# Kernel tuning notes

Hardware: AMD Instinct MI355X
Metric: run time of the kernel (lower is better)

The kernel has to match this reference:

```python
import jax, jax.numpy as jnp
import numpy as np

GROUPS = 32
NUM_HEADS = 8
EPS = 1e-5


def setup_inputs() -> dict:
    key = jax.random.key(0)
    ks = jax.random.split(key, 8)
    b, c, h, w = 2, 256, 64, 64
    x = jax.random.normal(ks[0], (b, c, h, w), dtype=jnp.float32)
    gn_w = jnp.ones((c,), dtype=jnp.float32)
    gn_b = jnp.zeros((c,), dtype=jnp.float32)
    qkv_w = jax.random.normal(ks[1], (3 * c, c), dtype=jnp.float32) * 0.02  # 1x1 conv
    qkv_b = jnp.zeros((3 * c,), dtype=jnp.float32)
    proj_w = jax.random.normal(ks[2], (c, c), dtype=jnp.float32) * 0.02  # 1x1 conv
    proj_b = jnp.zeros((c,), dtype=jnp.float32)
    return {"x": x, "gn_w": gn_w, "gn_b": gn_b, "qkv_w": qkv_w,
            "qkv_b": qkv_b, "proj_w": proj_w, "proj_b": proj_b}


def _group_norm(x, w, b):
    bsz, c, h, wd = x.shape
    xg = x.reshape(bsz, GROUPS, c // GROUPS, h * wd)
    mean = jnp.mean(xg, axis=(2, 3), keepdims=True)
    var = jnp.mean(jnp.square(xg - mean), axis=(2, 3), keepdims=True)
    xn = ((xg - mean) * jax.lax.rsqrt(var + EPS)).reshape(bsz, c, h, wd)
    return xn * w[None, :, None, None] + b[None, :, None, None]


def reference(x, gn_w, gn_b, qkv_w, qkv_b, proj_w, proj_b):
    b, c, h, w = x.shape
    hd = c // NUM_HEADS
    s = h * w
    xn = _group_norm(x, gn_w, gn_b)
    # 1x1 conv == channel matmul
    qkv = jnp.einsum('oc,bcs->bos', qkv_w, xn.reshape(b, c, s)) + qkv_b[None, :, None]
    qkv = qkv.reshape(b, 3, NUM_HEADS, hd, s)
    q, k, v = qkv[:, 0], qkv[:, 1], qkv[:, 2]  # (b, nh, hd, s)
    scale = 1.0 / jnp.sqrt(jnp.asarray(hd, dtype=x.dtype))
    scores = jnp.einsum('bhds,bhdt->bhst', q, k) * scale  # (b, nh, s, s)
    attn = jax.nn.softmax(scores, axis=-1)
    out = jnp.einsum('bhst,bhdt->bhds', attn, v)  # (b, nh, hd, s)
    out = out.reshape(b, c, h, w)
    out = jnp.einsum('oc,bcs->bos', proj_w, out.reshape(b, c, s)).reshape(b, c, h, w)
    out = out + proj_b[None, :, None, None]
    return out + x
```

## Files before the change

kernel.cpp:

```cpp
#include <hip/hip_runtime.h>
#include <hip/hip_bf16.h>

#define B_ 2
#define C_ 256
#define S_ 4096
#define NH 8
#define HD 32
#define EPSV 1e-5f
#define QSC2 0.25503487942324256f

typedef __bf16 bf16_t;
typedef bf16_t bf16x8 __attribute__((ext_vector_type(8)));
typedef float f32x4 __attribute__((ext_vector_type(4)));
typedef float f32x16 __attribute__((ext_vector_type(16)));
typedef int i32x2 __attribute__((ext_vector_type(2)));
typedef __hip_bfloat16 hbf;

__device__ inline unsigned cvtpk_bf16(float a, float b) {
  unsigned r;
  asm("v_cvt_pk_bf16_f32 %0, %1, %2" : "=v"(r) : "v"(a), "v"(b));
  return r;
}

#if __has_builtin(__builtin_amdgcn_exp2f)
#define EXP2R(x) __builtin_amdgcn_exp2f(x)
#else
#define EXP2R(x) exp2f(x)
#endif

__global__ __launch_bounds__(256) void f2bf_kernel(const float* __restrict__ src, hbf* __restrict__ dst, int n) {
  int i = blockIdx.x * 256 + threadIdx.x;
  if (i < n) dst[i] = __float2bfloat16(src[i]);
}

__global__ __launch_bounds__(256) void wfrag_kernel(const float* __restrict__ src, hbf* __restrict__ dst, int nchunks) {
  int i = blockIdx.x * 256 + threadIdx.x;
  if (i >= nchunks) return;
  int o = i >> 5, c8 = (i & 31) * 8;
  alignas(16) hbf tmp[8];
#pragma unroll
  for (int j = 0; j < 8; j++) tmp[j] = __float2bfloat16(src[(size_t)o * C_ + c8 + j]);
  *(uint4*)&dst[(((size_t)(o >> 5) * 16) + (c8 >> 4)) * 512 + (o & 31) * 16 + (c8 & 15)] = *(uint4*)tmp;
}

__global__ __launch_bounds__(256) void gn_stats(const float* __restrict__ x, float* __restrict__ stats) {
  int bg = blockIdx.x >> 3, chunk = blockIdx.x & 7;
  const float4* xp4 = (const float4*)(x + (size_t)bg * 8 * S_);
  float sum = 0.f, sumsq = 0.f;
#pragma unroll
  for (int p = 0; p < 4; p++) {
    int i = threadIdx.x + p * 256;
    int ch = i >> 7, s4 = i & 127;
    float4 v = xp4[ch * (S_ >> 2) + chunk * 128 + s4];
    sum += v.x + v.y + v.z + v.w;
    sumsq += v.x * v.x + v.y * v.y + v.z * v.z + v.w * v.w;
  }
#pragma unroll
  for (int off = 32; off > 0; off >>= 1) {
    sum += __shfl_down(sum, off);
    sumsq += __shfl_down(sumsq, off);
  }
  __shared__ float red[2][4];
  int wid = threadIdx.x >> 6;
  if ((threadIdx.x & 63) == 0) { red[0][wid] = sum; red[1][wid] = sumsq; }
  __syncthreads();
  if (threadIdx.x == 0) {
    stats[blockIdx.x * 2 + 0] = red[0][0] + red[0][1] + red[0][2] + red[0][3];
    stats[blockIdx.x * 2 + 1] = red[1][0] + red[1][1] + red[1][2] + red[1][3];
  }
}

__global__ __launch_bounds__(256) void gn_apply(const float* __restrict__ x, const float* __restrict__ gw,
                                                const float* __restrict__ gb, const float* __restrict__ stats,
                                                hbf* __restrict__ xn) {
  int bg = blockIdx.x >> 3, chunk = blockIdx.x & 7;
  int b = bg >> 5, g = bg & 31;
  const float* xp = x + (size_t)bg * 8 * S_;
  float sum = 0.f, sumsq = 0.f;
#pragma unroll
  for (int k = 0; k < 8; k++) {
    sum += stats[(bg * 8 + k) * 2 + 0];
    sumsq += stats[(bg * 8 + k) * 2 + 1];
  }
  const float inv_n = 1.f / (8 * S_);
  float mean = sum * inv_n;
  float rstd = rsqrtf(fmaxf(sumsq * inv_n - mean * mean, 0.f) + EPSV);
  float scv[8], shv[8];
#pragma unroll
  for (int c = 0; c < 8; c++) {
    scv[c] = gw[g * 8 + c] * rstd;
    shv[c] = gb[g * 8 + c] - mean * scv[c];
  }
#pragma unroll
  for (int p = 0; p < 2; p++) {
    int s = chunk * 512 + p * 256 + threadIdx.x;
    alignas(16) hbf tmp[8];
#pragma unroll
    for (int c = 0; c < 8; c++)
      tmp[c] = __float2bfloat16(xp[(size_t)c * S_ + s] * scv[c] + shv[c]);
    *(uint4*)&xn[(((size_t)b * (S_ >> 5) + (s >> 5)) * 16 + (g >> 1)) * 512 + (s & 31) * 16 + (g & 1) * 8] =
        *(uint4*)tmp;
  }
}

__global__ __launch_bounds__(512, 4) void qkv_gemm(const hbf* __restrict__ xn, const hbf* __restrict__ wf,
                                                   const float* __restrict__ bias,
                                                   hbf* __restrict__ qbuf, hbf* __restrict__ kg,
                                                   hbf* __restrict__ vg) {
  int bt = blockIdx.z;
  int m0 = blockIdx.x * 128;
  int n0 = blockIdx.y * 128;
  int tid = threadIdx.x, lane = tid & 63, w = tid >> 6;
  int wq = w & 3, wo = w >> 2;
  int l31 = lane & 31, hi = lane >> 5;
  const int loff = l31 * 16 + hi * 8;
  const hbf* ap = xn + ((size_t)bt * (S_ >> 5) + (m0 >> 5) + wq) * 8192;
  int oc0 = n0 + wo * 64;
  const hbf* bp0 = wf + (size_t)(oc0 >> 5) * 8192;
  const hbf* bp1 = bp0 + 8192;
  f32x16 acc0 = {0.f,0.f,0.f,0.f,0.f,0.f,0.f,0.f,0.f,0.f,0.f,0.f,0.f,0.f,0.f,0.f};
  f32x16 acc1 = acc0;
#pragma unroll 4
  for (int ks = 0; ks < 16; ++ks) {
    bf16x8 af = *(const bf16x8*)(ap + ks * 512 + loff);
    bf16x8 b0 = *(const bf16x8*)(bp0 + ks * 512 + loff);
    bf16x8 b1 = *(const bf16x8*)(bp1 + ks * 512 + loff);
    acc0 = __builtin_amdgcn_mfma_f32_32x32x16_bf16(af, b0, acc0, 0, 0, 0);
    acc1 = __builtin_amdgcn_mfma_f32_32x32x16_bf16(af, b1, acc1, 0, 0, 0);
  }
  int s_base = m0 + wq * 32;
#pragma unroll
  for (int ct = 0; ct < 2; ++ct) {
    f32x16 a = ct ? acc1 : acc0;
    int oc = oc0 + ct * 32;
    int o = oc + l31;
    float bs = bias[o];
    if (oc < 256) {
#pragma unroll
      for (int r = 0; r < 16; r++) {
        int s = s_base + (r & 3) + 8 * (r >> 2) + 4 * hi;
        qbuf[((size_t)bt * S_ + s) * C_ + o] = __float2bfloat16((a[r] + bs) * QSC2);
      }
    } else if (oc < 512) {
      int hh = (oc - 256) >> 5;
      const size_t khead = (size_t)(bt * NH + hh) * (S_ >> 5);
#pragma unroll
      for (int r = 0; r < 16; r++) {
        int s = s_base + (r & 3) + 8 * (r >> 2) + 4 * hi;
        kg[(khead + (s >> 5)) * 1024 + (l31 >> 4) * 512 + (s & 31) * 16 + (l31 & 15)] =
            __float2bfloat16(a[r] + bs);
      }
    } else {
      int hh = (oc - 512) >> 5;
      const size_t vhead = (size_t)(bt * NH + hh) * (S_ >> 4);
#pragma unroll
      for (int r = 0; r < 16; r++) {
        int s = s_base + (r & 3) + 8 * (r >> 2) + 4 * hi;
        vg[(vhead + (s >> 4)) * 512 + l31 * 16 + (s & 15)] = __float2bfloat16(a[r] + bs);
      }
    }
  }
}

__device__ inline void softmax_pv(f32x16 sc, bf16x8 va0, bf16x8 va1,
                                  f32x16& o_acc, float& l_run) {
#pragma unroll
  for (int i = 0; i < 16; i++) sc[i] = EXP2R(sc[i]);
  {
    float s0a = sc[0] + sc[1], s1a = sc[2] + sc[3], s2a = sc[4] + sc[5], s3a = sc[6] + sc[7];
    float s4a = sc[8] + sc[9], s5a = sc[10] + sc[11], s6a = sc[12] + sc[13], s7a = sc[14] + sc[15];
    s0a += s1a; s2a += s3a; s4a += s5a; s6a += s7a;
    s0a += s2a; s4a += s6a;
    l_run += s0a + s4a;
  }
#pragma unroll
  for (int kb = 0; kb < 2; kb++) {
    unsigned a0 = cvtpk_bf16(sc[kb * 8 + 0], sc[kb * 8 + 1]);
    unsigned b0 = cvtpk_bf16(sc[kb * 8 + 2], sc[kb * 8 + 3]);
    unsigned a1 = cvtpk_bf16(sc[kb * 8 + 4], sc[kb * 8 + 5]);
    unsigned b1 = cvtpk_bf16(sc[kb * 8 + 6], sc[kb * 8 + 7]);
    i32x2 ra = __builtin_amdgcn_permlane32_swap((int)a0, (int)a1, false, false);
    i32x2 rb = __builtin_amdgcn_permlane32_swap((int)b0, (int)b1, false, false);
    union { unsigned u[4]; bf16x8 v; } pf;
    pf.u[0] = (unsigned)ra[0]; pf.u[1] = (unsigned)rb[0];
    pf.u[2] = (unsigned)ra[1]; pf.u[3] = (unsigned)rb[1];
    o_acc = __builtin_amdgcn_mfma_f32_32x32x16_bf16(kb ? va1 : va0, pf.v, o_acc, 0, 0, 0);
  }
}

__global__ __launch_bounds__(512, 4) void attn_kernel(const hbf* __restrict__ qbuf, const hbf* __restrict__ kg,
                                                      const hbf* __restrict__ vg, hbf* __restrict__ attn_t) {
  int bid = blockIdx.x;
  int xcd = bid & 7, idx = bid >> 3;
  int combo = (xcd << 1) | (idx >> 6);
  int bt = combo >> 3, h = combo & 7;
  int s0 = (idx & 63) << 6;
  int tid = threadIdx.x, lane = tid & 63, w = tid >> 6;
  int wq = w & 1, wt = w >> 1;
  int l31 = lane & 31, hi = lane >> 5;
  const int loff = (l31 << 4) + (hi << 3);
  int qrow = s0 + wq * 32 + l31;
  bf16x8 qf0 = *(const bf16x8*)&qbuf[((size_t)bt * S_ + qrow) * C_ + h * HD + hi * 8];
  bf16x8 qf1 = *(const bf16x8*)&qbuf[((size_t)bt * S_ + qrow) * C_ + h * HD + 16 + hi * 8];
  f32x16 o_acc = {0.f,0.f,0.f,0.f,0.f,0.f,0.f,0.f,0.f,0.f,0.f,0.f,0.f,0.f,0.f,0.f};
  const f32x16 z16 = o_acc;
  float l_run = 0.f;
  const int tq0 = wt << 10;
  const hbf* kq = kg + ((size_t)(bt * NH + h) * (S_ >> 5) + (tq0 >> 5)) * 1024;
  const hbf* vq = vg + ((size_t)(bt * NH + h) * (S_ >> 4) + (tq0 >> 4)) * 512;
  bf16x8 kaB0 = *(const bf16x8*)(kq + loff);
  bf16x8 kaB1 = *(const bf16x8*)(kq + loff + 512);
  f32x16 scA = __builtin_amdgcn_mfma_f32_32x32x16_bf16(kaB0, qf0, z16, 0, 0, 0);
  scA = __builtin_amdgcn_mfma_f32_32x32x16_bf16(kaB1, qf1, scA, 0, 0, 0);
  kaB0 = *(const bf16x8*)(kq + loff + 1024);
  kaB1 = *(const bf16x8*)(kq + loff + 1536);
  bf16x8 vaA0 = *(const bf16x8*)(vq + loff);
  bf16x8 vaA1 = *(const bf16x8*)(vq + loff + 512);
  kq += 2048;
  vq += 1024;
  for (int j = 0; j < 15; ++j) {
    bf16x8 vaB0 = *(const bf16x8*)(vq + loff);
    bf16x8 vaB1 = *(const bf16x8*)(vq + loff + 512);
    bf16x8 knA0 = *(const bf16x8*)(kq + loff);
    bf16x8 knA1 = *(const bf16x8*)(kq + loff + 512);
    f32x16 scB = __builtin_amdgcn_mfma_f32_32x32x16_bf16(kaB0, qf0, z16, 0, 0, 0);
    scB = __builtin_amdgcn_mfma_f32_32x32x16_bf16(kaB1, qf1, scB, 0, 0, 0);
    kaB0 = *(const bf16x8*)(kq + loff + 1024);
    kaB1 = *(const bf16x8*)(kq + loff + 1536);
    softmax_pv(scA, vaA0, vaA1, o_acc, l_run);
    vaA0 = *(const bf16x8*)(vq + loff + 1024);
    vaA1 = *(const bf16x8*)(vq + loff + 1536);
    scA = __builtin_amdgcn_mfma_f32_32x32x16_bf16(knA0, qf0, z16, 0, 0, 0);
    scA = __builtin_amdgcn_mfma_f32_32x32x16_bf16(knA1, qf1, scA, 0, 0, 0);
    softmax_pv(scB, vaB0, vaB1, o_acc, l_run);
    kq += 2048; vq += 2048;
  }
  {
    bf16x8 vaB0 = *(const bf16x8*)(vq + loff);
    bf16x8 vaB1 = *(const bf16x8*)(vq + loff + 512);
    f32x16 scB = __builtin_amdgcn_mfma_f32_32x32x16_bf16(kaB0, qf0, z16, 0, 0, 0);
    scB = __builtin_amdgcn_mfma_f32_32x32x16_bf16(kaB1, qf1, scB, 0, 0, 0);
    softmax_pv(scA, vaA0, vaA1, o_acc, l_run);
    softmax_pv(scB, vaB0, vaB1, o_acc, l_run);
  }
  __shared__ f32x16 ored[6 * 64];
  __shared__ float lred[8 * 64];
  __syncthreads();
  lred[(w << 6) + lane] = l_run;
  if (wt > 0) ored[((w - 2) << 6) + lane] = o_acc;
  __syncthreads();
  if (wt == 0) {
    float l_tot = 0.f;
#pragma unroll
    for (int k = 0; k < 4; k++) {
      int wp = wq + 2 * k;
      l_tot += lred[(wp << 6) + l31] + lred[(wp << 6) + 32 + l31];
    }
    f32x16 o = o_acc;
#pragma unroll
    for (int k = 0; k < 3; k++) {
      f32x16 t2 = ored[((wq + 2 * k) << 6) + lane];
#pragma unroll
      for (int i = 0; i < 16; i++) o[i] += t2[i];
    }
    float inv_l = 1.0f / l_tot;
#pragma unroll
    for (int c2 = 0; c2 < 4; c2++) {
      alignas(8) hbf tmp[4];
#pragma unroll
      for (int r = 0; r < 4; r++) tmp[r] = __float2bfloat16(o[c2 * 4 + r] * inv_l);
      *(uint2*)&attn_t[((size_t)bt * S_ + qrow) * C_ + h * HD + c2 * 8 + hi * 4] = *(uint2*)tmp;
    }
  }
}

__global__ __launch_bounds__(256) void proj_gemm(const hbf* __restrict__ attn_t, const hbf* __restrict__ wb,
                                                 const float* __restrict__ bias, const float* __restrict__ x,
                                                 float* __restrict__ out) {
  int bt = blockIdx.z;
  int m0 = blockIdx.x * 64;
  int n0 = blockIdx.y * 64;
  const hbf* A = attn_t + (size_t)bt * S_ * C_;
  __shared__ hbf a_lds[64][72];
  __shared__ hbf b_lds[64][72];
  int tid = threadIdx.x, lane = tid & 63, wid = tid >> 6;
  int wm = (wid >> 1) * 32, wn = (wid & 1) * 32;
  f32x4 acc[2][2] = {};
  for (int k0 = 0; k0 < C_; k0 += 64) {
    __syncthreads();
    int r = tid >> 3, kk = (tid & 7) * 8;
#pragma unroll
    for (int p = 0; p < 2; p++) {
      *(bf16x8*)&a_lds[r + p * 32][kk] = *(const bf16x8*)&A[(size_t)(m0 + r + p * 32) * C_ + k0 + kk];
      *(bf16x8*)&b_lds[r + p * 32][kk] = *(const bf16x8*)&wb[(size_t)(n0 + r + p * 32) * C_ + k0 + kk];
    }
    __syncthreads();
#pragma unroll
    for (int kk2 = 0; kk2 < 64; kk2 += 32) {
      bf16x8 af[2], bfr[2];
#pragma unroll
      for (int mi = 0; mi < 2; mi++)
        af[mi] = *(const bf16x8*)&a_lds[wm + mi * 16 + (lane & 15)][kk2 + (lane >> 4) * 8];
#pragma unroll
      for (int ni = 0; ni < 2; ni++)
        bfr[ni] = *(const bf16x8*)&b_lds[wn + ni * 16 + (lane & 15)][kk2 + (lane >> 4) * 8];
#pragma unroll
      for (int mi = 0; mi < 2; mi++)
#pragma unroll
        for (int ni = 0; ni < 2; ni++)
          acc[mi][ni] = __builtin_amdgcn_mfma_f32_16x16x32_bf16(af[mi], bfr[ni], acc[mi][ni], 0, 0, 0);
    }
  }
#pragma unroll
  for (int mi = 0; mi < 2; mi++)
#pragma unroll
    for (int ni = 0; ni < 2; ni++) {
      int o = n0 + wn + ni * 16 + (lane & 15);
      int s = m0 + wm + mi * 16 + (lane >> 4) * 4;
      size_t base = ((size_t)bt * C_ + o) * S_ + s;
      float pb = bias[o];
      float4 xr = *(const float4*)&x[base];
      float4 res;
      res.x = acc[mi][ni][0] + pb + xr.x;
      res.y = acc[mi][ni][1] + pb + xr.y;
      res.z = acc[mi][ni][2] + pb + xr.z;
      res.w = acc[mi][ni][3] + pb + xr.w;
      *(float4*)&out[base] = res;
    }
}

extern "C" void kernel_launch(void* const* d_in, const int* in_sizes, int n_in,
                              void* d_out, int out_size, void* d_ws, size_t ws_size,
                              hipStream_t stream) {
  const float* x = (const float*)d_in[0];
  const float* gn_w = (const float*)d_in[1];
  const float* gn_b = (const float*)d_in[2];
  const float* qkv_w = (const float*)d_in[3];
  const float* qkv_b = (const float*)d_in[4];
  const float* proj_w = (const float*)d_in[5];
  const float* proj_b = (const float*)d_in[6];
  float* out = (float*)d_out;

  hbf* qkv_wf = (hbf*)d_ws;
  hbf* proj_w_bf = qkv_wf + 768 * 256;
  hbf* xn = proj_w_bf + 256 * 256;
  hbf* qbuf = xn + (size_t)B_ * S_ * C_;
  hbf* kg = qbuf + (size_t)B_ * S_ * C_;
  hbf* vg = kg + (size_t)B_ * S_ * C_;
  hbf* attn_t = vg + (size_t)B_ * S_ * C_;
  float* stats = (float*)(attn_t + (size_t)B_ * S_ * C_);

  dim3 blk(256);
  wfrag_kernel<<<(768 * 32 + 255) / 256, blk, 0, stream>>>(qkv_w, qkv_wf, 768 * 32);
  f2bf_kernel<<<(256 * 256 + 255) / 256, blk, 0, stream>>>(proj_w, proj_w_bf, 256 * 256);
  gn_stats<<<512, blk, 0, stream>>>(x, stats);
  gn_apply<<<512, blk, 0, stream>>>(x, gn_w, gn_b, stats, xn);
  qkv_gemm<<<dim3(32, 6, 2), dim3(512), 0, stream>>>(xn, qkv_wf, qkv_b, qbuf, kg, vg);
  attn_kernel<<<dim3(1024), dim3(512), 0, stream>>>(qbuf, kg, vg, attn_t);
  proj_gemm<<<dim3(64, 4, 2), blk, 0, stream>>>(attn_t, proj_w_bf, proj_b, x, out);
}
```

Baseline: 83.28 us.

## Merge weight prep and GN stats into one kernel; LDS-free proj GEMM with fragment-ordered weights

Fuses the qkv weight fragment conversion, the projection weight conversion and the group-norm statistics into a single launch, removing two kernel launches. The projection weights are now stored in the same fragment-major layout as the qkv weights. proj_gemm drops its LDS staging and barriers and feeds 32x32x16 MFMAs straight from global memory. This cuts launch overhead and LDS/sync cost, but the epilogue now does scalar, lane-strided stores and x reads instead of float4, which may hurt coalescing.

```diff
diff --git a/kernel.cpp b/kernel.cpp
--- a/kernel.cpp
+++ b/kernel.cpp
@@ -28,23 +28,28 @@
 #define EXP2R(x) exp2f(x)
 #endif
 
-__global__ __launch_bounds__(256) void f2bf_kernel(const float* __restrict__ src, hbf* __restrict__ dst, int n) {
-  int i = blockIdx.x * 256 + threadIdx.x;
-  if (i < n) dst[i] = __float2bfloat16(src[i]);
-}
-
-__global__ __launch_bounds__(256) void wfrag_kernel(const float* __restrict__ src, hbf* __restrict__ dst, int nchunks) {
-  int i = blockIdx.x * 256 + threadIdx.x;
-  if (i >= nchunks) return;
-  int o = i >> 5, c8 = (i & 31) * 8;
-  alignas(16) hbf tmp[8];
-#pragma unroll
-  for (int j = 0; j < 8; j++) tmp[j] = __float2bfloat16(src[(size_t)o * C_ + c8 + j]);
-  *(uint4*)&dst[(((size_t)(o >> 5) * 16) + (c8 >> 4)) * 512 + (o & 31) * 16 + (c8 & 15)] = *(uint4*)tmp;
-}
-
-__global__ __launch_bounds__(256) void gn_stats(const float* __restrict__ x, float* __restrict__ stats) {
-  int bg = blockIdx.x >> 3, chunk = blockIdx.x & 7;
+__global__ __launch_bounds__(256) void prep_kernel(const float* __restrict__ qkv_w,
+                                                   const float* __restrict__ proj_w,
+                                                   const float* __restrict__ x,
+                                                   hbf* __restrict__ qkv_wf, hbf* __restrict__ proj_wf,
+                                                   float* __restrict__ stats) {
+  int blk = blockIdx.x;
+  if (blk < 128) {
+    const float* src = (blk < 96) ? qkv_w : proj_w;
+    hbf* dst = (blk < 96) ? qkv_wf : proj_wf;
+    int i = (blk < 96 ? blk : blk - 96) * 256 + threadIdx.x;
+    int nchunks = (blk < 96) ? 768 * 32 : 256 * 32;
+    if (i < nchunks) {
+      int o = i >> 5, c8 = (i & 31) * 8;
+      alignas(16) hbf tmp[8];
+#pragma unroll
+      for (int j = 0; j < 8; j++) tmp[j] = __float2bfloat16(src[(size_t)o * C_ + c8 + j]);
+      *(uint4*)&dst[(((size_t)(o >> 5) * 16) + (c8 >> 4)) * 512 + (o & 31) * 16 + (c8 & 15)] = *(uint4*)tmp;
+    }
+    return;
+  }
+  int sb = blk - 128;
+  int bg = sb >> 3, chunk = sb & 7;
   const float4* xp4 = (const float4*)(x + (size_t)bg * 8 * S_);
   float sum = 0.f, sumsq = 0.f;
 #pragma unroll
@@ -65,8 +70,8 @@
   if ((threadIdx.x & 63) == 0) { red[0][wid] = sum; red[1][wid] = sumsq; }
   __syncthreads();
   if (threadIdx.x == 0) {
-    stats[blockIdx.x * 2 + 0] = red[0][0] + red[0][1] + red[0][2] + red[0][3];
-    stats[blockIdx.x * 2 + 1] = red[1][0] + red[1][1] + red[1][2] + red[1][3];
+    stats[sb * 2 + 0] = red[0][0] + red[0][1] + red[0][2] + red[0][3];
+    stats[sb * 2 + 1] = red[1][0] + red[1][1] + red[1][2] + red[1][3];
   }
 }
 
@@ -274,59 +279,34 @@
   }
 }
 
-__global__ __launch_bounds__(256) void proj_gemm(const hbf* __restrict__ attn_t, const hbf* __restrict__ wb,
+__global__ __launch_bounds__(256) void proj_gemm(const hbf* __restrict__ attn_t, const hbf* __restrict__ wf,
                                                  const float* __restrict__ bias, const float* __restrict__ x,
                                                  float* __restrict__ out) {
   int bt = blockIdx.z;
-  int m0 = blockIdx.x * 64;
-  int n0 = blockIdx.y * 64;
-  const hbf* A = attn_t + (size_t)bt * S_ * C_;
-  __shared__ hbf a_lds[64][72];
-  __shared__ hbf b_lds[64][72];
-  int tid = threadIdx.x, lane = tid & 63, wid = tid >> 6;
-  int wm = (wid >> 1) * 32, wn = (wid & 1) * 32;
-  f32x4 acc[2][2] = {};
-  for (int k0 = 0; k0 < C_; k0 += 64) {
-    __syncthreads();
-    int r = tid >> 3, kk = (tid & 7) * 8;
-#pragma unroll
-    for (int p = 0; p < 2; p++) {
-      *(bf16x8*)&a_lds[r + p * 32][kk] = *(const bf16x8*)&A[(size_t)(m0 + r + p * 32) * C_ + k0 + kk];
-      *(bf16x8*)&b_lds[r + p * 32][kk] = *(const bf16x8*)&wb[(size_t)(n0 + r + p * 32) * C_ + k0 + kk];
-    }
-    __syncthreads();
-#pragma unroll
-    for (int kk2 = 0; kk2 < 64; kk2 += 32) {
-      bf16x8 af[2], bfr[2];
-#pragma unroll
-      for (int mi = 0; mi < 2; mi++)
-        af[mi] = *(const bf16x8*)&a_lds[wm + mi * 16 + (lane & 15)][kk2 + (lane >> 4) * 8];
-#pragma unroll
-      for (int ni = 0; ni < 2; ni++)
-        bfr[ni] = *(const bf16x8*)&b_lds[wn + ni * 16 + (lane & 15)][kk2 + (lane >> 4) * 8];
-#pragma unroll
-      for (int mi = 0; mi < 2; mi++)
-#pragma unroll
-        for (int ni = 0; ni < 2; ni++)
-          acc[mi][ni] = __builtin_amdgcn_mfma_f32_16x16x32_bf16(af[mi], bfr[ni], acc[mi][ni], 0, 0, 0);
-    }
-  }
-#pragma unroll
-  for (int mi = 0; mi < 2; mi++)
-#pragma unroll
-    for (int ni = 0; ni < 2; ni++) {
-      int o = n0 + wn + ni * 16 + (lane & 15);
-      int s = m0 + wm + mi * 16 + (lane >> 4) * 4;
-      size_t base = ((size_t)bt * C_ + o) * S_ + s;
-      float pb = bias[o];
-      float4 xr = *(const float4*)&x[base];
-      float4 res;
-      res.x = acc[mi][ni][0] + pb + xr.x;
-      res.y = acc[mi][ni][1] + pb + xr.y;
-      res.z = acc[mi][ni][2] + pb + xr.z;
-      res.w = acc[mi][ni][3] + pb + xr.w;
-      *(float4*)&out[base] = res;
-    }
+  int s_blk = blockIdx.x * 64;
+  int o_blk = blockIdx.y * 64;
+  int tid = threadIdx.x, lane = tid & 63, w = tid >> 6;
+  int wo = w & 1, ws = w >> 1;
+  int l31 = lane & 31, hi = lane >> 5;
+  const int loff = l31 * 16 + hi * 8;
+  int o0 = o_blk + wo * 32;
+  int s0 = s_blk + ws * 32;
+  const hbf* ap = wf + (size_t)(o0 >> 5) * 8192;
+  const hbf* bp = attn_t + ((size_t)bt * S_ + s0 + l31) * C_ + hi * 8;
+  f32x16 acc = {0.f,0.f,0.f,0.f,0.f,0.f,0.f,0.f,0.f,0.f,0.f,0.f,0.f,0.f,0.f,0.f};
+#pragma unroll 4
+  for (int ks = 0; ks < 16; ++ks) {
+    bf16x8 af = *(const bf16x8*)(ap + ks * 512 + loff);
+    bf16x8 bf_ = *(const bf16x8*)(bp + ks * 16);
+    acc = __builtin_amdgcn_mfma_f32_32x32x16_bf16(af, bf_, acc, 0, 0, 0);
+  }
+  int s = s0 + l31;
+#pragma unroll
+  for (int r = 0; r < 16; r++) {
+    int o = o0 + (r & 3) + 8 * (r >> 2) + 4 * hi;
+    size_t idx = ((size_t)bt * C_ + o) * S_ + s;
+    out[idx] = acc[r] + bias[o] + x[idx];
+  }
 }
 
 extern "C" void kernel_launch(void* const* d_in, const int* in_sizes, int n_in,
@@ -342,8 +322,8 @@
   float* out = (float*)d_out;
 
   hbf* qkv_wf = (hbf*)d_ws;
-  hbf* proj_w_bf = qkv_wf + 768 * 256;
-  hbf* xn = proj_w_bf + 256 * 256;
+  hbf* proj_wf = qkv_wf + 768 * 256;
+  hbf* xn = proj_wf + 256 * 256;
   hbf* qbuf = xn + (size_t)B_ * S_ * C_;
   hbf* kg = qbuf + (size_t)B_ * S_ * C_;
   hbf* vg = kg + (size_t)B_ * S_ * C_;
@@ -351,11 +331,9 @@
   float* stats = (float*)(attn_t + (size_t)B_ * S_ * C_);
 
   dim3 blk(256);
-  wfrag_kernel<<<(768 * 32 + 255) / 256, blk, 0, stream>>>(qkv_w, qkv_wf, 768 * 32);
-  f2bf_kernel<<<(256 * 256 + 255) / 256, blk, 0, stream>>>(proj_w, proj_w_bf, 256 * 256);
-  gn_stats<<<512, blk, 0, stream>>>(x, stats);
+  prep_kernel<<<640, blk, 0, stream>>>(qkv_w, proj_w, x, qkv_wf, proj_wf, stats);
   gn_apply<<<512, blk, 0, stream>>>(x, gn_w, gn_b, stats, xn);
   qkv_gemm<<<dim3(32, 6, 2), dim3(512), 0, stream>>>(xn, qkv_wf, qkv_b, qbuf, kg, vg);
   attn_kernel<<<dim3(1024), dim3(512), 0, stream>>>(qbuf, kg, vg, attn_t);
-  proj_gemm<<<dim3(64, 4, 2), blk, 0, stream>>>(attn_t, proj_w_bf, proj_b, x, out);
-}
+  proj_gemm<<<dim3(64, 4, 2), blk, 0, stream>>>(attn_t, proj_wf, proj_b, x, out);
+}
```

Measured after the change: 79.22 us. -4.9%, faster.
